# Performance work log

Measured on AMD Instinct MI355X. Metric: run time of the kernel, lower is better.

The kernel has to match this reference:

```python
import jax, jax.numpy as jnp
import numpy as np

B, D, E, H, K = 8192, 1024, 8, 4096, 2

def setup_inputs() -> dict:
    key = jax.random.key(0)
    ks = jax.random.split(key, 7)
    s_in = 1.0 / np.sqrt(D)
    s_hid = 1.0 / np.sqrt(H)
    return {
        "z":  jax.random.normal(ks[0], (B, D), dtype=jnp.float32),
        "Wg": jax.random.uniform(ks[1], (D, E), jnp.float32, -s_in, s_in),
        "bg": jnp.zeros((E,), jnp.float32),
        "W1": jax.random.uniform(ks[2], (E, D, H), jnp.float32, -s_in, s_in),
        "b1": jax.random.uniform(ks[3], (E, H), jnp.float32, -s_in, s_in),
        "W2": jax.random.uniform(ks[4], (E, H, D), jnp.float32, -s_hid, s_hid),
        "b2": jax.random.uniform(ks[5], (E, D), jnp.float32, -s_hid, s_hid),
    }

def reference(z, Wg, bg, W1, b1, W2, b2):
    # gate: softmax over experts, then keep only top-k weights (no renorm,
    # matching the original which sums topw * expert(z))
    w = jax.nn.softmax(z @ Wg + bg, axis=-1)            # [B, E]
    topw, idx = jax.lax.top_k(w, K)                      # [B, K] each
    wmask = jnp.zeros_like(w).at[jnp.arange(B)[:, None], idx].set(topw)  # [B, E]
    # dense all-expert MLP, then weighted combine (same math as per-token loop)
    h = jax.nn.relu(jnp.einsum('bd,edh->beh', z, W1) + b1)   # [B, E, H]
    y = jnp.einsum('beh,ehd->bed', h, W2) + b2               # [B, E, D]
    out = jnp.einsum('be,bed->bd', wmask, y)                 # [B, D]
    return out
```

## Files before the change

### kernel.cpp

```cpp
#include <hip/hip_runtime.h>
#include <hip/hip_bf16.h>
#include <cstdint>
#include <cstddef>

#define BTOK  8192
#define DIM   1024
#define NEXP  8
#define NHID  4096
#define HHALF 2048
#define GATE_TOK 64

typedef __bf16 bf16x8 __attribute__((ext_vector_type(8)));
typedef float  floatx4 __attribute__((ext_vector_type(4)));

#define O_COUNTS 0
#define O_BASE   256
#define O_TOKB   1024
#define O_TOKW   (O_TOKB + (size_t)NEXP*BTOK*4)
#define O_CE     (O_TOKW + (size_t)NEXP*BTOK*4)
#define O_CP     (O_CE + (size_t)2*BTOK*4)
#define O_CW     (O_CP + (size_t)2*BTOK*4)
#define O_ZBF    (O_CW + (size_t)2*BTOK*4)
#define O_W1T    (O_ZBF + (size_t)BTOK*DIM*2)
#define O_W2T    (O_W1T + (size_t)NEXP*DIM*NHID*2)
#define O_HBUF   (O_W2T + (size_t)NEXP*DIM*NHID*2)
#define WS_BASE  (O_HBUF + (size_t)2*BTOK*HHALF*2)
#define O_YBUF   WS_BASE
#define WS_FULL  (O_YBUF + (size_t)2*BTOK*DIM*4)

__device__ __forceinline__ void gload_lds16(const void* g, void* l) {
  __builtin_amdgcn_global_load_lds(
      (const __attribute__((address_space(1))) void*)g,
      (__attribute__((address_space(3))) void*)l, 16, 0, 0);
}

__device__ __forceinline__ ushort f2bf(float x) {
  return __builtin_bit_cast(ushort, __float2bfloat16(x));
}

__global__ void k_zcnt(int* __restrict__ counts) {
  if (threadIdx.x < NEXP) counts[threadIdx.x] = 0;
}

__global__ void k_zout(float* __restrict__ out) {
  int i = blockIdx.x * blockDim.x + threadIdx.x;
  float4 z4 = {0.f, 0.f, 0.f, 0.f};
  float4* o = (float4*)out;
  int n = BTOK * DIM / 4;
  for (int j = i; j < n; j += gridDim.x * blockDim.x) o[j] = z4;
}

__global__ __launch_bounds__(256) void k_transpose(
    const float* __restrict__ src, __hip_bfloat16* __restrict__ dst, int R, int C) {
  __shared__ float tile[32][33];
  int zz = blockIdx.z;
  const float* s = src + (size_t)zz * R * C;
  __hip_bfloat16* d = dst + (size_t)zz * R * C;
  int c0 = blockIdx.x * 32, r0 = blockIdx.y * 32;
  int tx = threadIdx.x & 31, ty = threadIdx.x >> 5;
#pragma unroll
  for (int i = ty; i < 32; i += 8)
    tile[i][tx] = s[(size_t)(r0 + i) * C + c0 + tx];
  __syncthreads();
#pragma unroll
  for (int i = ty; i < 32; i += 8)
    d[(size_t)(c0 + i) * R + r0 + tx] = __float2bfloat16(tile[tx][i]);
}

__global__ __launch_bounds__(256) void k_gate(
    const float* __restrict__ z, const float* __restrict__ Wg,
    const float* __restrict__ bg, int* __restrict__ counts,
    int* __restrict__ tokb, float* __restrict__ tokw,
    int* __restrict__ ce, int* __restrict__ cp, float* __restrict__ cw,
    __hip_bfloat16* __restrict__ zbf) {
  __shared__ float wgT[NEXP * DIM];
  __shared__ int   le[2 * GATE_TOK];
  __shared__ float lw[2 * GATE_TOK];
  __shared__ int   lr[2 * GATE_TOK];
  __shared__ int   lcnt[NEXP];
  __shared__ int   gbase[NEXP];

  int tid = threadIdx.x;
  if (tid < NEXP) lcnt[tid] = 0;
#pragma unroll
  for (int e = 0; e < NEXP; e++)
    for (int d = tid; d < DIM; d += 256)
      wgT[e * DIM + d] = Wg[d * NEXP + e];
  __syncthreads();

  int lane = tid & 63;
  int wv = tid >> 6;
  int b0 = blockIdx.x * GATE_TOK;

  for (int t = 0; t < 16; t++) {
    int lt = wv * 16 + t;
    int b = b0 + lt;
    const float4* zr4 = (const float4*)(z + (size_t)b * DIM);
    float4 zv[4];
#pragma unroll
    for (int i = 0; i < 4; i++) zv[i] = zr4[lane + 64 * i];
    ushort4* zb4 = (ushort4*)((ushort*)zbf + (size_t)b * DIM);
#pragma unroll
    for (int i = 0; i < 4; i++) {
      ushort4 u;
      u.x = f2bf(zv[i].x); u.y = f2bf(zv[i].y);
      u.z = f2bf(zv[i].z); u.w = f2bf(zv[i].w);
      zb4[lane + 64 * i] = u;
    }
    float acc[NEXP];
#pragma unroll
    for (int e = 0; e < NEXP; e++) acc[e] = 0.f;
#pragma unroll
    for (int e = 0; e < NEXP; e++) {
      const float4* wg4 = (const float4*)(wgT + e * DIM);
#pragma unroll
      for (int i = 0; i < 4; i++) {
        float4 w4 = wg4[lane + 64 * i];
        acc[e] += zv[i].x * w4.x + zv[i].y * w4.y + zv[i].z * w4.z + zv[i].w * w4.w;
      }
    }
#pragma unroll
    for (int off = 32; off > 0; off >>= 1) {
#pragma unroll
      for (int e = 0; e < NEXP; e++) acc[e] += __shfl_down(acc[e], off);
    }
    if (lane == 0) {
      float mx = -1e30f;
#pragma unroll
      for (int e = 0; e < NEXP; e++) { acc[e] += bg[e]; mx = fmaxf(mx, acc[e]); }
      float s = 0.f;
#pragma unroll
      for (int e = 0; e < NEXP; e++) { acc[e] = expf(acc[e] - mx); s += acc[e]; }
      float inv = 1.f / s;
      int i1 = -1, i2 = -1; float v1 = -1.f, v2 = -1.f;
#pragma unroll
      for (int e = 0; e < NEXP; e++) {
        float w = acc[e] * inv;
        if (w > v1) { v2 = v1; i2 = i1; v1 = w; i1 = e; }
        else if (w > v2) { v2 = w; i2 = e; }
      }
      le[2 * lt] = i1;     lw[2 * lt] = v1;
      le[2 * lt + 1] = i2; lw[2 * lt + 1] = v2;
    }
  }
  __syncthreads();
  if (tid < 2 * GATE_TOK) lr[tid] = atomicAdd(&lcnt[le[tid]], 1);
  __syncthreads();
  if (tid < NEXP) gbase[tid] = atomicAdd(&counts[tid], lcnt[tid]);
  __syncthreads();
  if (tid < 2 * GATE_TOK) {
    int e = le[tid];
    int p = gbase[e] + lr[tid];
    int b = b0 + (tid >> 1);
    int slot = tid & 1;
    tokb[e * BTOK + p] = b;
    tokw[e * BTOK + p] = lw[tid];
    ce[2 * b + slot] = e;
    cp[2 * b + slot] = p;
    cw[2 * b + slot] = lw[tid];
  }
}

__global__ void k_base(const int* __restrict__ counts, int* __restrict__ base) {
  if (threadIdx.x == 0 && blockIdx.x == 0) {
    int s = 0;
    for (int e = 0; e < NEXP; e++) { base[e] = s; s += counts[e]; }
  }
}


#define STG(bb_, op_, SRC_, kh_, tt_) do {                                   \
    gload_lds16(SRC_[0] + (tt_) * 64 + (kh_) * 32,                           \
                &lds[bb_][op_][kh_][(0 * 128 + wv * 16) * 32]);              \
    gload_lds16(SRC_[1] + (tt_) * 64 + (kh_) * 32,                           \
                &lds[bb_][op_][kh_][(1 * 128 + wv * 16) * 32]);              \
  } while (0)

#define PH(cur_, kk_, ih_, STAGE_, WAIT_) do {                               \
    const ushort* Ab_ = &lds[cur_][0][kk_][0];                               \
    const ushort* Bb_ = &lds[cur_][1][kk_][0];                               \
    if (ih_ == 0) {                                                          \
      _Pragma("unroll")                                                      \
      for (int j_ = 0; j_ < 4; j_++)                                         \
        bfr[j_] = __builtin_bit_cast(bf16x8,                                 \
            *(const uint4*)(Bb_ + boff + j_ * 512));                         \
    }                                                                        \
    bf16x8 afr_[4];                                                          \
    _Pragma("unroll")                                                        \
    for (int i_ = 0; i_ < 4; i_++)                                           \
      afr_[i_] = __builtin_bit_cast(bf16x8,                                  \
          *(const uint4*)(Ab_ + aoff + ((ih_) * 4 + i_) * 512));             \
    STAGE_;                                                                  \
    __builtin_amdgcn_sched_barrier(0);                                       \
    WAIT_;                                                                   \
    __builtin_amdgcn_s_barrier();                                            \
    __builtin_amdgcn_sched_barrier(0);                                       \
    __builtin_amdgcn_s_setprio(1);                                           \
    _Pragma("unroll")                                                        \
    for (int i_ = 0; i_ < 4; i_++)                                           \
      _Pragma("unroll")                                                      \
      for (int j_ = 0; j_ < 4; j_++)                                         \
        acc[(ih_) * 4 + i_][j_] = __builtin_amdgcn_mfma_f32_16x16x32_bf16(   \
            afr_[i_], bfr[j_], acc[(ih_) * 4 + i_][j_], 0, 0, 0);            \
    __builtin_amdgcn_s_setprio(0);                                           \
    __builtin_amdgcn_sched_barrier(0);                                       \
    __builtin_amdgcn_s_barrier();                                            \
  } while (0)

#define VM6 asm volatile("s_waitcnt vmcnt(6)" ::: "memory")
#define VM0 asm volatile("s_waitcnt vmcnt(0)" ::: "memory")
#define NOP_ (void)0

__global__ __launch_bounds__(512, 2) void k_gemm1(
    const __hip_bfloat16* __restrict__ zbf, const __hip_bfloat16* __restrict__ w1t,
    const float* __restrict__ b1, const int* __restrict__ counts,
    const int* __restrict__ base, const int* __restrict__ tokb,
    __hip_bfloat16* __restrict__ hbuf, int hbase) {
  int e = blockIdx.z;
  int cnt = counts[e];
  if (cnt == 0) return;
  int n0 = blockIdx.y * 256;
  int gb = base[e];

  __shared__ __align__(16) ushort lds[2][2][2][256 * 32];

  int tid = threadIdx.x;
  int lane = tid & 63;
  int wv = tid >> 6;
  int wm = wv >> 2;
  int wn = wv & 3;
  int lrow = lane & 15;
  int quad = lane >> 4;
  int pc = quad ^ ((lrow >> 1) & 3);
  int aoff = (wm * 128 + lrow) * 32 + pc * 8;
  int boff = (wn * 64 + lrow) * 32 + pc * 8;

  const ushort* zb = (const ushort*)zbf;
  const ushort* w1 = (const ushort*)w1t;

  const ushort* srcB[2];
#pragma unroll
  for (int l = 0; l < 2; l++) {
    int r = l * 128 + wv * 16 + (lane >> 2);
    srcB[l] = w1 + (size_t)(e * NHID + hbase + n0 + r) * DIM
                 + (size_t)(((lane & 3) ^ ((r >> 1) & 3)) * 8);
  }

  const int NT = DIM / 64;

  for (int mt = blockIdx.x; mt * 256 < cnt; mt += gridDim.x) {
    int m0 = mt * 256;
    const ushort* srcA[2];
#pragma unroll
    for (int l = 0; l < 2; l++) {
      int r = l * 128 + wv * 16 + (lane >> 2);
      int m = m0 + r; if (m >= cnt) m = cnt - 1;
      srcA[l] = zb + (size_t)tokb[e * BTOK + m] * DIM
                   + (size_t)(((lane & 3) ^ ((r >> 1) & 3)) * 8);
    }

    STG(0, 0, srcA, 0, 0); STG(0, 1, srcB, 0, 0);
    STG(0, 0, srcA, 1, 0); STG(0, 1, srcB, 1, 0);
    STG(1, 1, srcB, 0, 1); STG(1, 0, srcA, 0, 1); STG(1, 1, srcB, 1, 1);
    VM6;
    __builtin_amdgcn_s_barrier();

    floatx4 acc[8][4];
#pragma unroll
    for (int i = 0; i < 8; i++)
#pragma unroll
      for (int j = 0; j < 4; j++) { floatx4 zf = {0.f,0.f,0.f,0.f}; acc[i][j] = zf; }
    bf16x8 bfr[4];

#pragma unroll 1
    for (int t = 0; t < NT - 2; ++t) {
      int cur = t & 1;
      PH(cur, 0, 0, STG(cur ^ 1, 0, srcA, 1, t + 1), NOP_);
      PH(cur, 0, 1, STG(cur, 1, srcB, 0, t + 2), NOP_);
      PH(cur, 1, 0, STG(cur, 0, srcA, 0, t + 2), NOP_);
      PH(cur, 1, 1, STG(cur, 1, srcB, 1, t + 2), VM6);
    }
    {
      int cur = (NT - 2) & 1;
      PH(cur, 0, 0, STG(cur ^ 1, 0, srcA, 1, NT - 1), NOP_);
      PH(cur, 0, 1, NOP_, NOP_);
      PH(cur, 1, 0, NOP_, NOP_);
      PH(cur, 1, 1, NOP_, VM0);
    }
    {
      int cur = (NT - 1) & 1;
      PH(cur, 0, 0, NOP_, NOP_);
      PH(cur, 0, 1, NOP_, NOP_);
      PH(cur, 1, 0, NOP_, NOP_);
      PH(cur, 1, 1, NOP_, NOP_);
    }

    float bias[4];
#pragma unroll
    for (int j = 0; j < 4; j++)
      bias[j] = b1[e * NHID + hbase + n0 + wn * 64 + j * 16 + lrow];
    ushort* hp = (ushort*)hbuf;
#pragma unroll
    for (int i = 0; i < 8; i++) {
      int mloc = wm * 128 + i * 16 + quad * 4;
#pragma unroll
      for (int r = 0; r < 4; r++) {
        int m = m0 + mloc + r;
        if (m < cnt) {
          ushort* hr = hp + (size_t)(gb + m) * HHALF;
#pragma unroll
          for (int j = 0; j < 4; j++) {
            float v = fmaxf(acc[i][j][r] + bias[j], 0.f);
            hr[n0 + wn * 64 + j * 16 + lrow] = f2bf(v);
          }
        }
      }
    }
  }
}

__global__ __launch_bounds__(512, 2) void k_gemm2(
    const __hip_bfloat16* __restrict__ hbuf, const __hip_bfloat16* __restrict__ w2t,
    const float* __restrict__ b2, const int* __restrict__ counts,
    const int* __restrict__ base, const int* __restrict__ tokb,
    const float* __restrict__ tokw, float* __restrict__ out,
    float* __restrict__ ybuf, int hbase, int pass) {
  int e = blockIdx.z;
  int cnt = counts[e];
  if (cnt == 0) return;
  int n0 = blockIdx.y * 256;
  int gb = base[e];

  __shared__ __align__(16) ushort lds[2][2][2][256 * 32];

  int tid = threadIdx.x;
  int lane = tid & 63;
  int wv = tid >> 6;
  int wm = wv >> 2;
  int wn = wv & 3;
  int lrow = lane & 15;
  int quad = lane >> 4;
  int pc = quad ^ ((lrow >> 1) & 3);
  int aoff = (wm * 128 + lrow) * 32 + pc * 8;
  int boff = (wn * 64 + lrow) * 32 + pc * 8;

  const ushort* hb = (const ushort*)hbuf;
  const ushort* w2 = (const ushort*)w2t;

  const ushort* srcB[2];
#pragma unroll
  for (int l = 0; l < 2; l++) {
    int r = l * 128 + wv * 16 + (lane >> 2);
    srcB[l] = w2 + (size_t)(e * DIM + n0 + r) * NHID + hbase
                 + (size_t)(((lane & 3) ^ ((r >> 1) & 3)) * 8);
  }

  const int NT = HHALF / 64;

  for (int mt = blockIdx.x; mt * 256 < cnt; mt += gridDim.x) {
    int m0 = mt * 256;
    const ushort* srcA[2];
#pragma unroll
    for (int l = 0; l < 2; l++) {
      int r = l * 128 + wv * 16 + (lane >> 2);
      int m = m0 + r; if (m >= cnt) m = cnt - 1;
      srcA[l] = hb + (size_t)(gb + m) * HHALF
                   + (size_t)(((lane & 3) ^ ((r >> 1) & 3)) * 8);
    }

    STG(0, 0, srcA, 0, 0); STG(0, 1, srcB, 0, 0);
    STG(0, 0, srcA, 1, 0); STG(0, 1, srcB, 1, 0);
    STG(1, 1, srcB, 0, 1); STG(1, 0, srcA, 0, 1); STG(1, 1, srcB, 1, 1);
    VM6;
    __builtin_amdgcn_s_barrier();

    floatx4 acc[8][4];
#pragma unroll
    for (int i = 0; i < 8; i++)
#pragma unroll
      for (int j = 0; j < 4; j++) { floatx4 zf = {0.f,0.f,0.f,0.f}; acc[i][j] = zf; }
    bf16x8 bfr[4];

#pragma unroll 1
    for (int t = 0; t < NT - 2; ++t) {
      int cur = t & 1;
      PH(cur, 0, 0, STG(cur ^ 1, 0, srcA, 1, t + 1), NOP_);
      PH(cur, 0, 1, STG(cur, 1, srcB, 0, t + 2), NOP_);
      PH(cur, 1, 0, STG(cur, 0, srcA, 0, t + 2), NOP_);
      PH(cur, 1, 1, STG(cur, 1, srcB, 1, t + 2), VM6);
    }
    {
      int cur = (NT - 2) & 1;
      PH(cur, 0, 0, STG(cur ^ 1, 0, srcA, 1, NT - 1), NOP_);
      PH(cur, 0, 1, NOP_, NOP_);
      PH(cur, 1, 0, NOP_, NOP_);
      PH(cur, 1, 1, NOP_, VM0);
    }
    {
      int cur = (NT - 1) & 1;
      PH(cur, 0, 0, NOP_, NOP_);
      PH(cur, 0, 1, NOP_, NOP_);
      PH(cur, 1, 0, NOP_, NOP_);
      PH(cur, 1, 1, NOP_, NOP_);
    }

    if (ybuf) {
      float bias[4];
#pragma unroll
      for (int j = 0; j < 4; j++)
        bias[j] = pass ? b2[e * DIM + n0 + wn * 64 + j * 16 + lrow] : 0.f;
#pragma unroll
      for (int i = 0; i < 8; i++) {
        int mloc = wm * 128 + i * 16 + quad * 4;
#pragma unroll
        for (int r = 0; r < 4; r++) {
          int m = m0 + mloc + r;
          if (m < cnt) {
            float* yr = ybuf + (size_t)(gb + m) * DIM;
#pragma unroll
            for (int j = 0; j < 4; j++) {
              int n = n0 + wn * 64 + j * 16 + lrow;
              if (pass == 0) yr[n] = acc[i][j][r];
              else           yr[n] += acc[i][j][r] + bias[j];
            }
          }
        }
      }
    } else {
#pragma unroll
      for (int i = 0; i < 8; i++) {
        int mloc = wm * 128 + i * 16 + quad * 4;
#pragma unroll
        for (int r = 0; r < 4; r++) {
          int m = m0 + mloc + r;
          if (m < cnt) {
            int tk  = tokb[e * BTOK + m];
            float w = tokw[e * BTOK + m];
#pragma unroll
            for (int j = 0; j < 4; j++) {
              int n = n0 + wn * 64 + j * 16 + lrow;
              float v = acc[i][j][r] + (pass ? b2[e * DIM + n] : 0.f);
              atomicAdd(&out[(size_t)tk * DIM + n], w * v);
            }
          }
        }
      }
    }
  }
}

__global__ __launch_bounds__(256) void k_combine(
    const float* __restrict__ ybuf, const int* __restrict__ base,
    const int* __restrict__ ce, const int* __restrict__ cp,
    const float* __restrict__ cw, float* __restrict__ out) {
  int b = blockIdx.x;
  int n = threadIdx.x * 4;
  int e1 = ce[2 * b], e2 = ce[2 * b + 1];
  int s1 = base[e1] + cp[2 * b];
  int s2 = base[e2] + cp[2 * b + 1];
  float w1 = cw[2 * b], w2 = cw[2 * b + 1];
  float4 a = *(const float4*)(ybuf + (size_t)s1 * DIM + n);
  float4 c = *(const float4*)(ybuf + (size_t)s2 * DIM + n);
  float4 o;
  o.x = w1 * a.x + w2 * c.x;
  o.y = w1 * a.y + w2 * c.y;
  o.z = w1 * a.z + w2 * c.z;
  o.w = w1 * a.w + w2 * c.w;
  *(float4*)(out + (size_t)b * DIM + n) = o;
}

extern "C" void kernel_launch(void* const* d_in, const int* in_sizes, int n_in,
                              void* d_out, int out_size, void* d_ws, size_t ws_size,
                              hipStream_t stream) {
  const float* z  = (const float*)d_in[0];
  const float* Wg = (const float*)d_in[1];
  const float* bg = (const float*)d_in[2];
  const float* W1 = (const float*)d_in[3];
  const float* b1 = (const float*)d_in[4];
  const float* W2 = (const float*)d_in[5];
  const float* b2 = (const float*)d_in[6];
  float* out = (float*)d_out;
  char* ws = (char*)d_ws;
  if (ws_size < WS_BASE) return;
  bool use_ybuf = ws_size >= WS_FULL;

  int*   counts = (int*)(ws + O_COUNTS);
  int*   base   = (int*)(ws + O_BASE);
  int*   tokb   = (int*)(ws + O_TOKB);
  float* tokw   = (float*)(ws + O_TOKW);
  int*   ce     = (int*)(ws + O_CE);
  int*   cp     = (int*)(ws + O_CP);
  float* cw     = (float*)(ws + O_CW);
  __hip_bfloat16* zbf  = (__hip_bfloat16*)(ws + O_ZBF);
  __hip_bfloat16* w1t  = (__hip_bfloat16*)(ws + O_W1T);
  __hip_bfloat16* w2t  = (__hip_bfloat16*)(ws + O_W2T);
  __hip_bfloat16* hbuf = (__hip_bfloat16*)(ws + O_HBUF);
  float* ybuf = use_ybuf ? (float*)(ws + O_YBUF) : nullptr;

  k_zcnt<<<1, 64, 0, stream>>>(counts);
  if (!use_ybuf) k_zout<<<512, 256, 0, stream>>>(out);
  k_transpose<<<dim3(NHID / 32, DIM / 32, NEXP), 256, 0, stream>>>(W1, w1t, DIM, NHID);
  k_transpose<<<dim3(DIM / 32, NHID / 32, NEXP), 256, 0, stream>>>(W2, w2t, NHID, DIM);
  k_gate<<<BTOK / GATE_TOK, 256, 0, stream>>>(z, Wg, bg, counts, tokb, tokw, ce, cp, cw, zbf);
  k_base<<<1, 64, 0, stream>>>(counts, base);
  for (int half = 0; half < 2; half++) {
    k_gemm1<<<dim3(8, HHALF / 256, NEXP), 512, 0, stream>>>(
        zbf, w1t, b1, counts, base, tokb, hbuf, half * HHALF);
    k_gemm2<<<dim3(8, DIM / 256, NEXP), 512, 0, stream>>>(
        hbuf, w2t, b2, counts, base, tokb, tokw, out, ybuf, half * HHALF, half);
  }
  if (use_ybuf)
    k_combine<<<BTOK, 256, 0, stream>>>(ybuf, base, ce, cp, cw, out);
}
```

Before: 948.9 us.

## Switch expert GEMMs to persistent work-stealing tiles with smaller M tiles and triple buffering

Replaces the fixed 3D grid (blocks per expert and N tile, looping over M tiles) with a persistent 512-block grid. Each block atomically grabs tile indices from a global counter and maps them to expert/M/N tiles via prefix sums computed in k_base. The M tile shrinks from 256 to 128, K steps shrink to 32 with a 3-stage LDS ring buffer, and occupancy rises to 4 blocks per CU. The aim is to fix load imbalance across experts with uneven token counts and improve latency hiding. In exchange it adds atomic and sync overhead per tile and lowers arithmetic intensity per tile.

```diff
diff --git a/kernel.cpp b/kernel.cpp
--- a/kernel.cpp
+++ b/kernel.cpp
@@ -9,6 +9,7 @@
 #define NHID  4096
 #define HHALF 2048
 #define GATE_TOK 64
+#define ABASE (128 * 32)
 
 typedef __bf16 bf16x8 __attribute__((ext_vector_type(8)));
 typedef float  floatx4 __attribute__((ext_vector_type(4)));
@@ -39,7 +40,7 @@
 }
 
 __global__ void k_zcnt(int* __restrict__ counts) {
-  if (threadIdx.x < NEXP) counts[threadIdx.x] = 0;
+  if (threadIdx.x < 12) counts[threadIdx.x] = 0;
 }
 
 __global__ void k_zout(float* __restrict__ out) {
@@ -165,34 +166,38 @@
   if (threadIdx.x == 0 && blockIdx.x == 0) {
     int s = 0;
     for (int e = 0; e < NEXP; e++) { base[e] = s; s += counts[e]; }
-  }
-}
-
-
-#define STG(bb_, op_, SRC_, kh_, tt_) do {                                   \
-    gload_lds16(SRC_[0] + (tt_) * 64 + (kh_) * 32,                           \
-                &lds[bb_][op_][kh_][(0 * 128 + wv * 16) * 32]);              \
-    gload_lds16(SRC_[1] + (tt_) * 64 + (kh_) * 32,                           \
-                &lds[bb_][op_][kh_][(1 * 128 + wv * 16) * 32]);              \
+    int a = 0, b = 0;
+    base[8] = 0; base[17] = 0;
+    for (int e = 0; e < NEXP; e++) {
+      int mt = (counts[e] + 127) >> 7;
+      a += mt * 8; b += mt * 4;
+      base[9 + e] = a; base[18 + e] = b;
+    }
+  }
+}
+
+
+#define STG3(nxt_, tt_) do {                                                 \
+    gload_lds16(srcA  + (tt_) * 32, &lds[nxt_][(wv * 16) * 32]);             \
+    gload_lds16(srcB0 + (tt_) * 32, &lds[nxt_][ABASE + (wv * 16) * 32]);     \
+    gload_lds16(srcB1 + (tt_) * 32, &lds[nxt_][ABASE + (128 + wv * 16) * 32]);\
   } while (0)
 
-#define PH(cur_, kk_, ih_, STAGE_, WAIT_) do {                               \
-    const ushort* Ab_ = &lds[cur_][0][kk_][0];                               \
-    const ushort* Bb_ = &lds[cur_][1][kk_][0];                               \
-    if (ih_ == 0) {                                                          \
-      _Pragma("unroll")                                                      \
-      for (int j_ = 0; j_ < 4; j_++)                                         \
-        bfr[j_] = __builtin_bit_cast(bf16x8,                                 \
-            *(const uint4*)(Bb_ + boff + j_ * 512));                         \
-    }                                                                        \
-    bf16x8 afr_[4];                                                          \
+#define PH3(cur_, STG_, VM_) do {                                            \
+    const ushort* Ab_ = &lds[cur_][0];                                       \
+    const ushort* Bb_ = &lds[cur_][ABASE];                                   \
+    bf16x8 afr_[4], bfr_[4];                                                 \
+    _Pragma("unroll")                                                        \
+    for (int j_ = 0; j_ < 4; j_++)                                           \
+      bfr_[j_] = __builtin_bit_cast(bf16x8,                                  \
+          *(const uint4*)(Bb_ + boff + j_ * 512));                           \
     _Pragma("unroll")                                                        \
     for (int i_ = 0; i_ < 4; i_++)                                           \
       afr_[i_] = __builtin_bit_cast(bf16x8,                                  \
-          *(const uint4*)(Ab_ + aoff + ((ih_) * 4 + i_) * 512));             \
-    STAGE_;                                                                  \
+          *(const uint4*)(Ab_ + aoff + i_ * 512));                           \
+    STG_;                                                                    \
     __builtin_amdgcn_sched_barrier(0);                                       \
-    WAIT_;                                                                   \
+    VM_;                                                                     \
     __builtin_amdgcn_s_barrier();                                            \
     __builtin_amdgcn_sched_barrier(0);                                       \
     __builtin_amdgcn_s_setprio(1);                                           \
@@ -200,29 +205,25 @@
     for (int i_ = 0; i_ < 4; i_++)                                           \
       _Pragma("unroll")                                                      \
       for (int j_ = 0; j_ < 4; j_++)                                         \
-        acc[(ih_) * 4 + i_][j_] = __builtin_amdgcn_mfma_f32_16x16x32_bf16(   \
-            afr_[i_], bfr[j_], acc[(ih_) * 4 + i_][j_], 0, 0, 0);            \
+        acc[i_][j_] = __builtin_amdgcn_mfma_f32_16x16x32_bf16(               \
+            afr_[i_], bfr_[j_], acc[i_][j_], 0, 0, 0);                       \
     __builtin_amdgcn_s_setprio(0);                                           \
     __builtin_amdgcn_sched_barrier(0);                                       \
     __builtin_amdgcn_s_barrier();                                            \
   } while (0)
 
-#define VM6 asm volatile("s_waitcnt vmcnt(6)" ::: "memory")
-#define VM0 asm volatile("s_waitcnt vmcnt(0)" ::: "memory")
+#define VM3  asm volatile("s_waitcnt vmcnt(3)" ::: "memory")
+#define VM0  asm volatile("s_waitcnt vmcnt(0)" ::: "memory")
 #define NOP_ (void)0
 
-__global__ __launch_bounds__(512, 2) void k_gemm1(
+__global__ __launch_bounds__(512, 4) void k_gemm1(
     const __hip_bfloat16* __restrict__ zbf, const __hip_bfloat16* __restrict__ w1t,
     const float* __restrict__ b1, const int* __restrict__ counts,
     const int* __restrict__ base, const int* __restrict__ tokb,
-    __hip_bfloat16* __restrict__ hbuf, int hbase) {
-  int e = blockIdx.z;
-  int cnt = counts[e];
-  if (cnt == 0) return;
-  int n0 = blockIdx.y * 256;
-  int gb = base[e];
-
-  __shared__ __align__(16) ushort lds[2][2][2][256 * 32];
+    __hip_bfloat16* __restrict__ hbuf, int hbase,
+    const int* __restrict__ tp, int* __restrict__ steal) {
+  __shared__ __align__(16) ushort lds[3][(128 + 256) * 32];
+  __shared__ int sh_g;
 
   int tid = threadIdx.x;
   int lane = tid & 63;
@@ -232,68 +233,57 @@
   int lrow = lane & 15;
   int quad = lane >> 4;
   int pc = quad ^ ((lrow >> 1) & 3);
-  int aoff = (wm * 128 + lrow) * 32 + pc * 8;
+  int aoff = (wm * 64 + lrow) * 32 + pc * 8;
   int boff = (wn * 64 + lrow) * 32 + pc * 8;
+  int srow = wv * 16 + (lane >> 2);
+  int sswz = ((lane & 3) ^ ((srow >> 1) & 3)) * 8;
 
   const ushort* zb = (const ushort*)zbf;
   const ushort* w1 = (const ushort*)w1t;
-
-  const ushort* srcB[2];
-#pragma unroll
-  for (int l = 0; l < 2; l++) {
-    int r = l * 128 + wv * 16 + (lane >> 2);
-    srcB[l] = w1 + (size_t)(e * NHID + hbase + n0 + r) * DIM
-                 + (size_t)(((lane & 3) ^ ((r >> 1) & 3)) * 8);
-  }
-
-  const int NT = DIM / 64;
-
-  for (int mt = blockIdx.x; mt * 256 < cnt; mt += gridDim.x) {
-    int m0 = mt * 256;
-    const ushort* srcA[2];
-#pragma unroll
-    for (int l = 0; l < 2; l++) {
-      int r = l * 128 + wv * 16 + (lane >> 2);
-      int m = m0 + r; if (m >= cnt) m = cnt - 1;
-      srcA[l] = zb + (size_t)tokb[e * BTOK + m] * DIM
-                   + (size_t)(((lane & 3) ^ ((r >> 1) & 3)) * 8);
-    }
-
-    STG(0, 0, srcA, 0, 0); STG(0, 1, srcB, 0, 0);
-    STG(0, 0, srcA, 1, 0); STG(0, 1, srcB, 1, 0);
-    STG(1, 1, srcB, 0, 1); STG(1, 0, srcA, 0, 1); STG(1, 1, srcB, 1, 1);
-    VM6;
+  const int NT = DIM / 32;
+  int TT = tp[8];
+
+  for (;;) {
+    if (tid == 0) sh_g = atomicAdd(steal, 1);
+    __syncthreads();
+    int g = sh_g;
+    if (g >= TT) break;
+
+    int e = 0;
+    while (g >= tp[e + 1]) e++;
+    int local = g - tp[e];
+    int mte = (tp[e + 1] - tp[e]) >> 3;
+    int nt = local / mte;
+    int mtl = local - nt * mte;
+    int m0 = mtl * 128, n0 = nt * 256;
+    int cnt = counts[e], gb = base[e];
+
+    int m = m0 + srow; if (m >= cnt) m = cnt - 1;
+    const ushort* srcA = zb + (size_t)tokb[e * BTOK + m] * DIM + sswz;
+    const ushort* srcB0 = w1 + (size_t)(e * NHID + hbase + n0 + srow) * DIM + sswz;
+    const ushort* srcB1 = w1 + (size_t)(e * NHID + hbase + n0 + 128 + srow) * DIM + sswz;
+
+    STG3(0, 0);
+    STG3(1, 1);
+    VM3;
     __builtin_amdgcn_s_barrier();
 
-    floatx4 acc[8][4];
-#pragma unroll
-    for (int i = 0; i < 8; i++)
+    floatx4 acc[4][4];
+#pragma unroll
+    for (int i = 0; i < 4; i++)
 #pragma unroll
       for (int j = 0; j < 4; j++) { floatx4 zf = {0.f,0.f,0.f,0.f}; acc[i][j] = zf; }
-    bf16x8 bfr[4];
-
+
+    int cur = 0;
 #pragma unroll 1
     for (int t = 0; t < NT - 2; ++t) {
-      int cur = t & 1;
-      PH(cur, 0, 0, STG(cur ^ 1, 0, srcA, 1, t + 1), NOP_);
-      PH(cur, 0, 1, STG(cur, 1, srcB, 0, t + 2), NOP_);
-      PH(cur, 1, 0, STG(cur, 0, srcA, 0, t + 2), NOP_);
-      PH(cur, 1, 1, STG(cur, 1, srcB, 1, t + 2), VM6);
-    }
-    {
-      int cur = (NT - 2) & 1;
-      PH(cur, 0, 0, STG(cur ^ 1, 0, srcA, 1, NT - 1), NOP_);
-      PH(cur, 0, 1, NOP_, NOP_);
-      PH(cur, 1, 0, NOP_, NOP_);
-      PH(cur, 1, 1, NOP_, VM0);
-    }
-    {
-      int cur = (NT - 1) & 1;
-      PH(cur, 0, 0, NOP_, NOP_);
-      PH(cur, 0, 1, NOP_, NOP_);
-      PH(cur, 1, 0, NOP_, NOP_);
-      PH(cur, 1, 1, NOP_, NOP_);
-    }
+      int nxt = cur + 2; if (nxt >= 3) nxt -= 3;
+      PH3(cur, STG3(nxt, t + 2), VM3);
+      cur = (cur == 2) ? 0 : cur + 1;
+    }
+    PH3(cur, NOP_, VM0);
+    cur = (cur == 2) ? 0 : cur + 1;
+    PH3(cur, NOP_, NOP_);
 
     float bias[4];
 #pragma unroll
@@ -301,13 +291,13 @@
       bias[j] = b1[e * NHID + hbase + n0 + wn * 64 + j * 16 + lrow];
     ushort* hp = (ushort*)hbuf;
 #pragma unroll
-    for (int i = 0; i < 8; i++) {
-      int mloc = wm * 128 + i * 16 + quad * 4;
+    for (int i = 0; i < 4; i++) {
+      int mloc = wm * 64 + i * 16 + quad * 4;
 #pragma unroll
       for (int r = 0; r < 4; r++) {
-        int m = m0 + mloc + r;
-        if (m < cnt) {
-          ushort* hr = hp + (size_t)(gb + m) * HHALF;
+        int mm = m0 + mloc + r;
+        if (mm < cnt) {
+          ushort* hr = hp + (size_t)(gb + mm) * HHALF;
 #pragma unroll
           for (int j = 0; j < 4; j++) {
             float v = fmaxf(acc[i][j][r] + bias[j], 0.f);
@@ -316,22 +306,19 @@
         }
       }
     }
-  }
-}
-
-__global__ __launch_bounds__(512, 2) void k_gemm2(
+    __syncthreads();
+  }
+}
+
+__global__ __launch_bounds__(512, 4) void k_gemm2(
     const __hip_bfloat16* __restrict__ hbuf, const __hip_bfloat16* __restrict__ w2t,
     const float* __restrict__ b2, const int* __restrict__ counts,
     const int* __restrict__ base, const int* __restrict__ tokb,
     const float* __restrict__ tokw, float* __restrict__ out,
-    float* __restrict__ ybuf, int hbase, int pass) {
-  int e = blockIdx.z;
-  int cnt = counts[e];
-  if (cnt == 0) return;
-  int n0 = blockIdx.y * 256;
-  int gb = base[e];
-
-  __shared__ __align__(16) ushort lds[2][2][2][256 * 32];
+    float* __restrict__ ybuf, int hbase, int pass,
+    const int* __restrict__ tp, int* __restrict__ steal) {
+  __shared__ __align__(16) ushort lds[3][(128 + 256) * 32];
+  __shared__ int sh_g;
 
   int tid = threadIdx.x;
   int lane = tid & 63;
@@ -341,68 +328,57 @@
   int lrow = lane & 15;
   int quad = lane >> 4;
   int pc = quad ^ ((lrow >> 1) & 3);
-  int aoff = (wm * 128 + lrow) * 32 + pc * 8;
+  int aoff = (wm * 64 + lrow) * 32 + pc * 8;
   int boff = (wn * 64 + lrow) * 32 + pc * 8;
+  int srow = wv * 16 + (lane >> 2);
+  int sswz = ((lane & 3) ^ ((srow >> 1) & 3)) * 8;
 
   const ushort* hb = (const ushort*)hbuf;
   const ushort* w2 = (const ushort*)w2t;
-
-  const ushort* srcB[2];
-#pragma unroll
-  for (int l = 0; l < 2; l++) {
-    int r = l * 128 + wv * 16 + (lane >> 2);
-    srcB[l] = w2 + (size_t)(e * DIM + n0 + r) * NHID + hbase
-                 + (size_t)(((lane & 3) ^ ((r >> 1) & 3)) * 8);
-  }
-
-  const int NT = HHALF / 64;
-
-  for (int mt = blockIdx.x; mt * 256 < cnt; mt += gridDim.x) {
-    int m0 = mt * 256;
-    const ushort* srcA[2];
-#pragma unroll
-    for (int l = 0; l < 2; l++) {
-      int r = l * 128 + wv * 16 + (lane >> 2);
-      int m = m0 + r; if (m >= cnt) m = cnt - 1;
-      srcA[l] = hb + (size_t)(gb + m) * HHALF
-                   + (size_t)(((lane & 3) ^ ((r >> 1) & 3)) * 8);
-    }
-
-    STG(0, 0, srcA, 0, 0); STG(0, 1, srcB, 0, 0);
-    STG(0, 0, srcA, 1, 0); STG(0, 1, srcB, 1, 0);
-    STG(1, 1, srcB, 0, 1); STG(1, 0, srcA, 0, 1); STG(1, 1, srcB, 1, 1);
-    VM6;
+  const int NT = HHALF / 32;
+  int TT = tp[8];
+
+  for (;;) {
+    if (tid == 0) sh_g = atomicAdd(steal, 1);
+    __syncthreads();
+    int g = sh_g;
+    if (g >= TT) break;
+
+    int e = 0;
+    while (g >= tp[e + 1]) e++;
+    int local = g - tp[e];
+    int mte = (tp[e + 1] - tp[e]) >> 2;
+    int nt = local / mte;
+    int mtl = local - nt * mte;
+    int m0 = mtl * 128, n0 = nt * 256;
+    int cnt = counts[e], gb = base[e];
+
+    int m = m0 + srow; if (m >= cnt) m = cnt - 1;
+    const ushort* srcA = hb + (size_t)(gb + m) * HHALF + sswz;
+    const ushort* srcB0 = w2 + (size_t)(e * DIM + n0 + srow) * NHID + hbase + sswz;
+    const ushort* srcB1 = w2 + (size_t)(e * DIM + n0 + 128 + srow) * NHID + hbase + sswz;
+
+    STG3(0, 0);
+    STG3(1, 1);
+    VM3;
     __builtin_amdgcn_s_barrier();
 
-    floatx4 acc[8][4];
-#pragma unroll
-    for (int i = 0; i < 8; i++)
+    floatx4 acc[4][4];
+#pragma unroll
+    for (int i = 0; i < 4; i++)
 #pragma unroll
       for (int j = 0; j < 4; j++) { floatx4 zf = {0.f,0.f,0.f,0.f}; acc[i][j] = zf; }
-    bf16x8 bfr[4];
-
+
+    int cur = 0;
 #pragma unroll 1
     for (int t = 0; t < NT - 2; ++t) {
-      int cur = t & 1;
-      PH(cur, 0, 0, STG(cur ^ 1, 0, srcA, 1, t + 1), NOP_);
-      PH(cur, 0, 1, STG(cur, 1, srcB, 0, t + 2), NOP_);
-      PH(cur, 1, 0, STG(cur, 0, srcA, 0, t + 2), NOP_);
-      PH(cur, 1, 1, STG(cur, 1, srcB, 1, t + 2), VM6);
-    }
-    {
-      int cur = (NT - 2) & 1;
-      PH(cur, 0, 0, STG(cur ^ 1, 0, srcA, 1, NT - 1), NOP_);
-      PH(cur, 0, 1, NOP_, NOP_);
-      PH(cur, 1, 0, NOP_, NOP_);
-      PH(cur, 1, 1, NOP_, VM0);
-    }
-    {
-      int cur = (NT - 1) & 1;
-      PH(cur, 0, 0, NOP_, NOP_);
-      PH(cur, 0, 1, NOP_, NOP_);
-      PH(cur, 1, 0, NOP_, NOP_);
-      PH(cur, 1, 1, NOP_, NOP_);
-    }
+      int nxt = cur + 2; if (nxt >= 3) nxt -= 3;
+      PH3(cur, STG3(nxt, t + 2), VM3);
+      cur = (cur == 2) ? 0 : cur + 1;
+    }
+    PH3(cur, NOP_, VM0);
+    cur = (cur == 2) ? 0 : cur + 1;
+    PH3(cur, NOP_, NOP_);
 
     if (ybuf) {
       float bias[4];
@@ -410,13 +386,13 @@
       for (int j = 0; j < 4; j++)
         bias[j] = pass ? b2[e * DIM + n0 + wn * 64 + j * 16 + lrow] : 0.f;
 #pragma unroll
-      for (int i = 0; i < 8; i++) {
-        int mloc = wm * 128 + i * 16 + quad * 4;
+      for (int i = 0; i < 4; i++) {
+        int mloc = wm * 64 + i * 16 + quad * 4;
 #pragma unroll
         for (int r = 0; r < 4; r++) {
-          int m = m0 + mloc + r;
-          if (m < cnt) {
-            float* yr = ybuf + (size_t)(gb + m) * DIM;
+          int mm = m0 + mloc + r;
+          if (mm < cnt) {
+            float* yr = ybuf + (size_t)(gb + mm) * DIM;
 #pragma unroll
             for (int j = 0; j < 4; j++) {
               int n = n0 + wn * 64 + j * 16 + lrow;
@@ -428,14 +404,14 @@
       }
     } else {
 #pragma unroll
-      for (int i = 0; i < 8; i++) {
-        int mloc = wm * 128 + i * 16 + quad * 4;
+      for (int i = 0; i < 4; i++) {
+        int mloc = wm * 64 + i * 16 + quad * 4;
 #pragma unroll
         for (int r = 0; r < 4; r++) {
-          int m = m0 + mloc + r;
-          if (m < cnt) {
-            int tk  = tokb[e * BTOK + m];
-            float w = tokw[e * BTOK + m];
+          int mm = m0 + mloc + r;
+          if (mm < cnt) {
+            int tk  = tokb[e * BTOK + mm];
+            float w = tokw[e * BTOK + mm];
 #pragma unroll
             for (int j = 0; j < 4; j++) {
               int n = n0 + wn * 64 + j * 16 + lrow;
@@ -446,6 +422,7 @@
         }
       }
     }
+    __syncthreads();
   }
 }
 
@@ -504,10 +481,12 @@
   k_gate<<<BTOK / GATE_TOK, 256, 0, stream>>>(z, Wg, bg, counts, tokb, tokw, ce, cp, cw, zbf);
   k_base<<<1, 64, 0, stream>>>(counts, base);
   for (int half = 0; half < 2; half++) {
-    k_gemm1<<<dim3(8, HHALF / 256, NEXP), 512, 0, stream>>>(
-        zbf, w1t, b1, counts, base, tokb, hbuf, half * HHALF);
-    k_gemm2<<<dim3(8, DIM / 256, NEXP), 512, 0, stream>>>(
-        hbuf, w2t, b2, counts, base, tokb, tokw, out, ybuf, half * HHALF, half);
+    k_gemm1<<<512, 512, 0, stream>>>(
+        zbf, w1t, b1, counts, base, tokb, hbuf, half * HHALF,
+        base + 8, counts + 8 + half * 2);
+    k_gemm2<<<512, 512, 0, stream>>>(
+        hbuf, w2t, b2, counts, base, tokb, tokw, out, ybuf, half * HHALF, half,
+        base + 17, counts + 9 + half * 2);
   }
   if (use_ybuf)
     k_combine<<<BTOK, 256, 0, stream>>>(ybuf, base, ce, cp, cw, out);
```

Measured after the change: 913.5 us. -3.7%, faster.
